# Kernel tuning notes

Measured on AMD Instinct MI355X. Metric: run time of the kernel, lower is better.

## Reference

```python
import jax, jax.numpy as jnp
import numpy as np

TAU = 0.75

def normalize_W(W):
    n = jnp.linalg.norm(W)
    n = jax.nn.relu(n - 1.0) + 1.0
    return W / n

def setup_inputs() -> dict:
    key = jax.random.key(0)
    ks = jax.random.split(key, 14)
    C_in, C_out, K = 64, 128, 3
    B, L = 32, 4096
    nh = 64
    chunk_in_d = C_out * K            # 384
    D = C_in * (K + 2 * (C_out // C_in))  # 448
    r = lambda k, shp, s=1.0: jax.random.normal(k, shp, dtype=jnp.float32) * s
    W = normalize_W(r(ks[4], (D, 32)))
    return {
        "x": r(ks[0], (B, C_in, L)),
        "conv_weight": r(ks[1], (C_out, C_in, K), 0.1),
        "bias_param": r(ks[2], (C_out,), 0.1),
        "grads": r(ks[3], (C_out * C_in * K,), 0.1),
        "W": W,
        "ctrl_w": r(ks[5], (nh, chunk_in_d), 0.05),
        "ctrl_b": r(ks[6], (nh,), 0.05),
        "cw_w": r(ks[7], (K, nh), 0.05),
        "cw_b": r(ks[8], (K,), 0.05),
        "cb_w": r(ks[9], (C_out // C_in, nh), 0.05),
        "cb_b": r(ks[10], (C_out // C_in,), 0.05),
        "cf_w": r(ks[11], (C_out // C_in, nh), 0.05),
        "cf_b": r(ks[12], (C_out // C_in,), 0.05),
        "trigger": 1,
    }

def fw_chunks(grads, W, ctrl_w, ctrl_b, cw_w, cw_b, cb_w, cb_b, cf_w, cf_b, trigger, n_chunks):
    g = grads.reshape(n_chunks, -1)                    # (C_in, C_out*K)
    rep = jax.nn.silu(g @ ctrl_w.T + ctrl_b)           # (C_in, nh)
    w = rep @ cw_w.T + cw_b                            # (C_in, K)
    b = rep @ cb_w.T + cb_b                            # (C_in, C_out/C_in)
    f = rep @ cf_w.T + cf_b                            # (C_in, C_out/C_in)
    q = jnp.concatenate([w.ravel(), b.ravel(), f.ravel()])  # (D,)  first call: no q_ema
    W_upd = W
    if trigger == 1:  # codebook attention / top-k / scatter-EMA path
        dim = w.shape[0]
        att = jax.nn.softmax(q @ W / 0.5)              # (32,)
        v, idx = jax.lax.top_k(att, 2)
        ww = W[:, idx]                                 # (D, 2)
        old_w = ww @ idx.astype(jnp.float32)[:, None]  # (D, 1) -- indices used as weights, as in source
        s_att = jnp.zeros((att.shape[0],), jnp.float32).at[idx].set(v)
        W_contrib = old_w @ s_att[None, :]             # (D, 32)
        mask = jnp.ones(W.shape, jnp.float32).at[:, idx].set(TAU)
        W_upd = normalize_W(mask * W + (1.0 - mask) * W_contrib)
        nw, nb, nf = w.shape[1], b.shape[1], f.shape[1]
        o_w = old_w[: nw * dim]
        o_b = old_w[nw * dim : (nw + nb) * dim]
        o_f = old_w[-nf * dim :]
        w = TAU * w + (1.0 - TAU) * o_w.reshape(w.shape)
        b = TAU * b + (1.0 - TAU) * o_b.reshape(b.shape)
        f = TAU * f + (1.0 - TAU) * o_f.reshape(f.shape)
    f = f.reshape(-1)[None, :, None]                   # (1, C_out, 1)
    return w[None], b.reshape(-1), f, W_upd

def reference(x, conv_weight, bias_param, grads, W, ctrl_w, ctrl_b, cw_w, cw_b, cb_w, cb_b, cf_w, cf_b, trigger):
    n_chunks = conv_weight.shape[1]  # in_channels
    w, b, f, W_upd = fw_chunks(grads, W, ctrl_w, ctrl_b, cw_w, cw_b, cb_w, cb_b, cf_w, cf_b, trigger, n_chunks)
    cw = conv_weight * w                               # (C_out, C_in, K)
    pad = ((conv_weight.shape[2] - 1) * 1 + 1) // 2    # receptive_field // 2
    conv_out = jax.lax.conv_general_dilated(
        x, cw, window_strides=(1,), padding=[(pad, pad)], rhs_dilation=(1,),
        dimension_numbers=("NCH", "OIH", "NCH"))
    conv_out = conv_out + (bias_param * b)[None, :, None]
    out = f * conv_out                                 # (B, C_out, L)
    return out, W_upd
```

## Files before the change

### kernel.cpp

```cpp
#include <hip/hip_runtime.h>
#include <hip/hip_bf16.h>
#include <math.h>

#define TAU 0.75f

typedef _Float16 half8 __attribute__((ext_vector_type(8)));
typedef float    f32x4 __attribute__((ext_vector_type(4)));

#define LDS_BARRIER() do {                                   \
    asm volatile("s_waitcnt lgkmcnt(0)" ::: "memory");       \
    __builtin_amdgcn_s_barrier();                            \
    asm volatile("" ::: "memory");                           \
} while (0)

#define WS_Q     0
#define WS_NORM2 448
#define WS_SCALE 449
#define WS_V01   450
#define WS_I01   452
#define WS_WQ    456
#define WS_FSC   648
#define WS_BADD  776
#define WS_OW    904
#define WS_WF16  1352

__global__ __launch_bounds__(256) void k1_rep_q(
    const float* __restrict__ grads, const float* __restrict__ ctrl_w,
    const float* __restrict__ ctrl_b,
    const float* __restrict__ cw_w, const float* __restrict__ cw_b,
    const float* __restrict__ cb_w, const float* __restrict__ cb_b,
    const float* __restrict__ cf_w, const float* __restrict__ cf_b,
    const float* __restrict__ W, float* __restrict__ ws)
{
    const int t = threadIdx.x;
    if (blockIdx.x == 64) {
        __shared__ float red[256];
        float ss = 0.f;
        for (int e = t; e < 3584; e += 256) {
            const float4 w4 = ((const float4*)W)[e];
            ss += w4.x * w4.x + w4.y * w4.y + w4.z * w4.z + w4.w * w4.w;
        }
        red[t] = ss; __syncthreads();
        for (int s = 128; s > 0; s >>= 1) { if (t < s) red[t] += red[t + s]; __syncthreads(); }
        if (t == 0) ws[WS_NORM2] = red[0];
        return;
    }
    const int c = blockIdx.x;
    __shared__ float gS[384];
    __shared__ float repS[64];
    if (t < 96) ((float4*)gS)[t] = ((const float4*)(grads + c * 384))[t];
    __syncthreads();
    {
        const int h = t >> 2, sub = t & 3;
        const float4* wa = (const float4*)(ctrl_w + h * 384) + sub * 24;
        const float4* ga = (const float4*)gS + sub * 24;
        float dot = 0.f;
        #pragma unroll
        for (int d = 0; d < 24; d++) {
            const float4 a = ga[d], b = wa[d];
            dot += a.x * b.x + a.y * b.y + a.z * b.z + a.w * b.w;
        }
        dot += __shfl_xor(dot, 1);
        dot += __shfl_xor(dot, 2);
        if (sub == 0) {
            const float z = dot + ctrl_b[h];
            repS[h] = z / (1.f + expf(-z));
        }
    }
    __syncthreads();
    if (t < 7) {
        const float* wv; float bias; int e;
        if (t < 3)      { wv = cw_w + t * 64;       bias = cw_b[t];     e = 3 * c + t; }
        else if (t < 5) { const int j = t - 3; wv = cb_w + j * 64; bias = cb_b[j]; e = 192 + 2 * c + j; }
        else            { const int j = t - 5; wv = cf_w + j * 64; bias = cf_b[j]; e = 320 + 2 * c + j; }
        float dot = 0.f;
        #pragma unroll 8
        for (int h = 0; h < 64; h++) dot += repS[h] * wv[h];
        ws[WS_Q + e] = dot + bias;
    }
}

__global__ __launch_bounds__(256) void k2_small(
    const float* __restrict__ W, const float* __restrict__ bias_param,
    const int* __restrict__ trigger, float* __restrict__ ws)
{
    __shared__ float qS[448], owS[448], sS[32], sW[4][32], red[256];
    __shared__ int   idxS[2];
    __shared__ float vS[2];
    const int t = threadIdx.x;
    const int wv = t >> 6, lane = t & 63;
    const int trig = trigger[0];

    for (int e = t; e < 448; e += 256) qS[e] = ws[WS_Q + e];
    __syncthreads();

    {
        const int m = lane & 31, half = lane >> 5;
        float s = 0.f;
        const int base = wv * 112;
        #pragma unroll 4
        for (int it = 0; it < 56; it++) {
            const int d = base + it * 2 + half;
            s += qS[d] * W[d * 32 + m];
        }
        s += __shfl_xor(s, 32);
        if (lane < 32) sW[wv][lane] = s;
    }
    __syncthreads();
    if (t < 32) sS[t] = 2.f * (sW[0][t] + sW[1][t] + sW[2][t] + sW[3][t]);
    __syncthreads();
    if (t == 0) {
        float mx = sS[0];
        for (int m = 1; m < 32; m++) mx = fmaxf(mx, sS[m]);
        float sum = 0.f; float att[32];
        for (int m = 0; m < 32; m++) { att[m] = expf(sS[m] - mx); sum += att[m]; }
        const float inv = 1.f / sum;
        int i0 = 0; float v0 = att[0];
        for (int m = 1; m < 32; m++) if (att[m] > v0) { v0 = att[m]; i0 = m; }
        int i1 = -1; float v1 = -1.f;
        for (int m = 0; m < 32; m++) { if (m == i0) continue; if (att[m] > v1) { v1 = att[m]; i1 = m; } }
        idxS[0] = i0; idxS[1] = i1; vS[0] = v0 * inv; vS[1] = v1 * inv;
    }
    __syncthreads();
    const int i0 = idxS[0], i1 = idxS[1];
    const float v0 = vS[0], v1 = vS[1];

    float corr = 0.f;
    for (int d = t; d < 448; d += 256) {
        const float w0 = W[d * 32 + i0], w1 = W[d * 32 + i1];
        const float ow = (trig == 1) ? (w0 * (float)i0 + w1 * (float)i1) : 0.f;
        owS[d] = ow;
        if (trig == 1) {
            const float n0 = TAU * w0 + 0.25f * ow * v0;
            const float n1 = TAU * w1 + 0.25f * ow * v1;
            corr += n0 * n0 - w0 * w0 + n1 * n1 - w1 * w1;
        }
    }
    red[t] = corr; __syncthreads();
    for (int s = 128; s > 0; s >>= 1) { if (t < s) red[t] += red[t + s]; __syncthreads(); }
    if (t == 0) {
        const float n = sqrtf(fmaxf(ws[WS_NORM2] + red[0], 0.f));
        ws[WS_SCALE] = 1.f / fmaxf(n, 1.f);
        ws[WS_V01] = v0; ws[WS_V01 + 1] = v1;
        ((int*)ws)[WS_I01] = i0; ((int*)ws)[WS_I01 + 1] = i1;
    }

    if (t < 192) ws[WS_WQ + t] = (trig == 1) ? (TAU * qS[t] + 0.25f * owS[t]) : qS[t];
    for (int o = t; o < 128; o += 256) {
        float bb = qS[192 + o], ff = qS[320 + o];
        if (trig == 1) {
            bb = TAU * bb + 0.25f * owS[192 + o];
            ff = TAU * ff + 0.25f * owS[320 + o];
        }
        ws[WS_FSC + o]  = ff;
        ws[WS_BADD + o] = ff * bias_param[o] * bb;
    }
    for (int d = t; d < 448; d += 256) ws[WS_OW + d] = owS[d];
}

__global__ __launch_bounds__(256) void k3_finalize(
    const float* __restrict__ W, const float* __restrict__ conv_weight,
    const int* __restrict__ trigger, const float* __restrict__ ws,
    float* __restrict__ W_out, _Float16* __restrict__ wf_out)
{
    const int g = blockIdx.x * 256 + threadIdx.x;
    const int trig = trigger[0];
    if (g < 14336) {
        const float wv = W[g];
        float wn = wv;
        if (trig == 1) {
            const int d = g >> 5, m = g & 31;
            const int i0 = ((const int*)ws)[WS_I01], i1 = ((const int*)ws)[WS_I01 + 1];
            if (m == i0)      wn = TAU * wv + 0.25f * ws[WS_OW + d] * ws[WS_V01];
            else if (m == i1) wn = TAU * wv + 0.25f * ws[WS_OW + d] * ws[WS_V01 + 1];
            wn *= ws[WS_SCALE];
        }
        W_out[g] = wn;
    } else {
        const int e2 = g - 14336;
        const int o   = e2 / 192;
        const int rem = e2 - o * 192;
        const int i   = rem / 3;
        const int kk  = rem - i * 3;
        wf_out[(kk * 128 + o) * 64 + i] = (_Float16)(conv_weight[e2] * ws[WS_WQ + rem]);
    }
}

__global__ __launch_bounds__(256, 4) void conv_mfma(
    const float* __restrict__ x, const _Float16* __restrict__ wf,
    const float* __restrict__ fsc, const float* __restrict__ badd,
    float* __restrict__ out)
{
    __shared__ __align__(16) _Float16 xs[2][66 * 72];

    const int t    = threadIdx.x;
    const int wv   = t >> 6;
    const int lane = t & 63;
    const int lrow = lane & 15;
    const int lgrp = lane >> 4;
    const int b    = blockIdx.x >> 5;
    const int l0   = (blockIdx.x & 31) * 128;
    const int obase = wv * 32;

    const float* xb = x + (size_t)b * 64 * 4096;
    const int ci = t & 3;
    const int ir = t >> 2;
    const int ei = t & 63;
    const int side = (t >> 6) & 1;

    half8 Wf[2][2][3];
    #pragma unroll
    for (int of = 0; of < 2; of++)
        #pragma unroll
        for (int ch = 0; ch < 2; ch++)
            #pragma unroll
            for (int kk = 0; kk < 3; kk++)
                Wf[of][ch][kk] = *(const half8*)(wf + ((kk * 128 + obase + of * 16 + lrow) * 64 + ch * 32 + lgrp * 8));

    float4 xr0[4]; float xe0 = 0.f;
    float4 xr1[4]; float xe1 = 0.f;

    {
        const int lb = l0;
        #pragma unroll
        for (int j = 0; j < 4; j++)
            xr0[j] = *(const float4*)(xb + (size_t)ir * 4096 + lb + ci * 16 + j * 4);
        if (t < 128) {
            const int l = side ? (lb + 64) : (lb - 1);
            if (l >= 0 && l < 4096) xe0 = xb[(size_t)ei * 4096 + l];
        }
    }
    {
        _Float16* buf = xs[0];
        #pragma unroll
        for (int j = 0; j < 4; j++) {
            _Float16* p = buf + (ci * 16 + j * 4 + 1) * 72 + ir;
            p[0]   = (_Float16)xr0[j].x;
            p[72]  = (_Float16)xr0[j].y;
            p[144] = (_Float16)xr0[j].z;
            p[216] = (_Float16)xr0[j].w;
        }
        if (t < 128) buf[(side ? 65 : 0) * 72 + ei] = (_Float16)xe0;
    }
    {
        const int lb = l0 + 64;
        #pragma unroll
        for (int j = 0; j < 4; j++)
            xr1[j] = *(const float4*)(xb + (size_t)ir * 4096 + lb + ci * 16 + j * 4);
        if (t < 128) {
            const int l = side ? (lb + 64) : (lb - 1);
            if (l >= 0 && l < 4096) xe1 = xb[(size_t)ei * 4096 + l];
        }
    }
    LDS_BARRIER();

    #pragma unroll
    for (int tile = 0; tile < 2; tile++) {
        const _Float16* buf = xs[tile];
        const int lb = l0 + tile * 64;

        f32x4 acc[2][4];
        #pragma unroll
        for (int of = 0; of < 2; of++)
            #pragma unroll
            for (int lf = 0; lf < 4; lf++) acc[of][lf] = (f32x4)0.f;

        #pragma unroll
        for (int ch = 0; ch < 2; ch++) {
            #pragma unroll
            for (int kk = 0; kk < 3; kk++) {
                half8 Xf[4];
                #pragma unroll
                for (int lf = 0; lf < 4; lf++)
                    Xf[lf] = *(const half8*)(buf + (lf * 16 + lrow + kk) * 72 + ch * 32 + lgrp * 8);
                #pragma unroll
                for (int of = 0; of < 2; of++)
                    #pragma unroll
                    for (int lf = 0; lf < 4; lf++)
                        acc[of][lf] = __builtin_amdgcn_mfma_f32_16x16x32_f16(Xf[lf], Wf[of][ch][kk], acc[of][lf], 0, 0, 0);
            }
        }

        #pragma unroll
        for (int of = 0; of < 2; of++) {
            const int o = obase + of * 16 + lrow;
            const float fs = fsc[o], ba = badd[o];
            float* orow = out + ((size_t)(b * 128 + o)) * 4096 + lb + lgrp * 4;
            #pragma unroll
            for (int lf = 0; lf < 4; lf++) {
                float4 r;
                r.x = fs * acc[of][lf][0] + ba;
                r.y = fs * acc[of][lf][1] + ba;
                r.z = fs * acc[of][lf][2] + ba;
                r.w = fs * acc[of][lf][3] + ba;
                *(float4*)(orow + lf * 16) = r;
            }
        }

        if (tile == 0) {
            _Float16* buf1 = xs[1];
            #pragma unroll
            for (int j = 0; j < 4; j++) {
                _Float16* p = buf1 + (ci * 16 + j * 4 + 1) * 72 + ir;
                p[0]   = (_Float16)xr1[j].x;
                p[72]  = (_Float16)xr1[j].y;
                p[144] = (_Float16)xr1[j].z;
                p[216] = (_Float16)xr1[j].w;
            }
            if (t < 128) buf1[(side ? 65 : 0) * 72 + ei] = (_Float16)xe1;
            LDS_BARRIER();
        }
    }
}

extern "C" void kernel_launch(void* const* d_in, const int* in_sizes, int n_in,
                              void* d_out, int out_size, void* d_ws, size_t ws_size,
                              hipStream_t stream) {
    const float* x           = (const float*)d_in[0];
    const float* conv_weight = (const float*)d_in[1];
    const float* bias_param  = (const float*)d_in[2];
    const float* grads       = (const float*)d_in[3];
    const float* W           = (const float*)d_in[4];
    const float* ctrl_w      = (const float*)d_in[5];
    const float* ctrl_b      = (const float*)d_in[6];
    const float* cw_w        = (const float*)d_in[7];
    const float* cw_b        = (const float*)d_in[8];
    const float* cb_w        = (const float*)d_in[9];
    const float* cb_b        = (const float*)d_in[10];
    const float* cf_w        = (const float*)d_in[11];
    const float* cf_b        = (const float*)d_in[12];
    const int*   trigger     = (const int*)d_in[13];

    float* out   = (float*)d_out;
    float* W_out = out + (size_t)32 * 128 * 4096;
    float* ws    = (float*)d_ws;
    _Float16* wfp = (_Float16*)(ws + WS_WF16);
    float* fsc   = ws + WS_FSC;
    float* badd  = ws + WS_BADD;

    k1_rep_q<<<65, 256, 0, stream>>>(grads, ctrl_w, ctrl_b, cw_w, cw_b,
                                     cb_w, cb_b, cf_w, cf_b, W, ws);
    k2_small<<<1, 256, 0, stream>>>(W, bias_param, trigger, ws);
    k3_finalize<<<152, 256, 0, stream>>>(W, conv_weight, trigger, ws, W_out, wfp);
    conv_mfma<<<1024, 256, 0, stream>>>(x, wfp, fsc, badd, out);
}
```

Measured before the change: 46.51 us.

## Process four L-tiles per conv block with a rolling double-buffered LDS pipeline

Each conv block now covers 256 positions (four 64-wide tiles) instead of 128, and the grid is halved to 512 blocks. A ping-pong pipeline loads the next tile's x from global memory into registers while the current tile is computed, then writes it to the other LDS buffer. The fsc/badd loads are hoisted out of the tile loop. The aim is to amortise the per-block weight-fragment loads and prologue, at the cost of fewer blocks (launch bound lowered to 2) and more registers, which may reduce occupancy and latency hiding on a bandwidth-bound kernel.

```diff
diff --git a/kernel.cpp b/kernel.cpp
--- a/kernel.cpp
+++ b/kernel.cpp
@@ -186,20 +186,20 @@
     }
 }
 
-__global__ __launch_bounds__(256, 4) void conv_mfma(
+__global__ __launch_bounds__(256, 2) void conv_mfma(
     const float* __restrict__ x, const _Float16* __restrict__ wf,
     const float* __restrict__ fsc, const float* __restrict__ badd,
     float* __restrict__ out)
 {
     __shared__ __align__(16) _Float16 xs[2][66 * 72];
 
-    const int t    = threadIdx.x;
-    const int wv   = t >> 6;
-    const int lane = t & 63;
-    const int lrow = lane & 15;
-    const int lgrp = lane >> 4;
-    const int b    = blockIdx.x >> 5;
-    const int l0   = (blockIdx.x & 31) * 128;
+    const int t     = threadIdx.x;
+    const int wv    = t >> 6;
+    const int lane  = t & 63;
+    const int lrow  = lane & 15;
+    const int lgrp  = lane >> 4;
+    const int b     = blockIdx.x >> 4;
+    const int lbase = (blockIdx.x & 15) * 256;
     const int obase = wv * 32;
 
     const float* xb = x + (size_t)b * 64 * 4096;
@@ -217,100 +217,100 @@
             for (int kk = 0; kk < 3; kk++)
                 Wf[of][ch][kk] = *(const half8*)(wf + ((kk * 128 + obase + of * 16 + lrow) * 64 + ch * 32 + lgrp * 8));
 
-    float4 xr0[4]; float xe0 = 0.f;
-    float4 xr1[4]; float xe1 = 0.f;
-
-    {
-        const int lb = l0;
-        #pragma unroll
-        for (int j = 0; j < 4; j++)
-            xr0[j] = *(const float4*)(xb + (size_t)ir * 4096 + lb + ci * 16 + j * 4);
-        if (t < 128) {
-            const int l = side ? (lb + 64) : (lb - 1);
-            if (l >= 0 && l < 4096) xe0 = xb[(size_t)ei * 4096 + l];
-        }
-    }
-    {
-        _Float16* buf = xs[0];
-        #pragma unroll
-        for (int j = 0; j < 4; j++) {
-            _Float16* p = buf + (ci * 16 + j * 4 + 1) * 72 + ir;
-            p[0]   = (_Float16)xr0[j].x;
-            p[72]  = (_Float16)xr0[j].y;
-            p[144] = (_Float16)xr0[j].z;
-            p[216] = (_Float16)xr0[j].w;
-        }
-        if (t < 128) buf[(side ? 65 : 0) * 72 + ei] = (_Float16)xe0;
-    }
-    {
-        const int lb = l0 + 64;
-        #pragma unroll
-        for (int j = 0; j < 4; j++)
-            xr1[j] = *(const float4*)(xb + (size_t)ir * 4096 + lb + ci * 16 + j * 4);
-        if (t < 128) {
-            const int l = side ? (lb + 64) : (lb - 1);
-            if (l >= 0 && l < 4096) xe1 = xb[(size_t)ei * 4096 + l];
-        }
-    }
+    float fs_[2], ba_[2];
+    #pragma unroll
+    for (int of = 0; of < 2; of++) {
+        const int o = obase + of * 16 + lrow;
+        fs_[of] = fsc[o]; ba_[of] = badd[o];
+    }
+
+    float4 xrA[4], xrB[4];
+    float  xeA = 0.f, xeB = 0.f;
+
+#define STAGE_LOAD(xr, xe, lb) do {                                          \
+    _Pragma("unroll")                                                        \
+    for (int j = 0; j < 4; j++)                                              \
+        (xr)[j] = *(const float4*)(xb + (size_t)ir * 4096 + (lb) + ci * 16 + j * 4); \
+    (xe) = 0.f;                                                              \
+    if (t < 128) {                                                           \
+        const int l_ = side ? ((lb) + 64) : ((lb) - 1);                      \
+        if (l_ >= 0 && l_ < 4096) (xe) = xb[(size_t)ei * 4096 + l_];         \
+    }                                                                        \
+} while (0)
+
+#define STAGE_WRITE(buf, xr, xe) do {                                        \
+    _Pragma("unroll")                                                        \
+    for (int j = 0; j < 4; j++) {                                            \
+        _Float16* p_ = (buf) + (ci * 16 + j * 4 + 1) * 72 + ir;              \
+        p_[0]   = (_Float16)(xr)[j].x;                                       \
+        p_[72]  = (_Float16)(xr)[j].y;                                       \
+        p_[144] = (_Float16)(xr)[j].z;                                       \
+        p_[216] = (_Float16)(xr)[j].w;                                       \
+    }                                                                        \
+    if (t < 128) (buf)[(side ? 65 : 0) * 72 + ei] = (_Float16)(xe);          \
+} while (0)
+
+#define COMPUTE_STORE(buf, lb) do {                                          \
+    f32x4 acc[2][4];                                                         \
+    _Pragma("unroll")                                                        \
+    for (int of = 0; of < 2; of++)                                           \
+        _Pragma("unroll")                                                    \
+        for (int lf = 0; lf < 4; lf++) acc[of][lf] = (f32x4)0.f;             \
+    _Pragma("unroll")                                                        \
+    for (int ch = 0; ch < 2; ch++) {                                         \
+        _Pragma("unroll")                                                    \
+        for (int kk = 0; kk < 3; kk++) {                                     \
+            half8 Xf[4];                                                     \
+            _Pragma("unroll")                                                \
+            for (int lf = 0; lf < 4; lf++)                                   \
+                Xf[lf] = *(const half8*)((buf) + (lf * 16 + lrow + kk) * 72 + ch * 32 + lgrp * 8); \
+            _Pragma("unroll")                                                \
+            for (int of = 0; of < 2; of++)                                   \
+                _Pragma("unroll")                                            \
+                for (int lf = 0; lf < 4; lf++)                               \
+                    acc[of][lf] = __builtin_amdgcn_mfma_f32_16x16x32_f16(Xf[lf], Wf[of][ch][kk], acc[of][lf], 0, 0, 0); \
+        }                                                                    \
+    }                                                                        \
+    _Pragma("unroll")                                                        \
+    for (int of = 0; of < 2; of++) {                                         \
+        const int o_ = obase + of * 16 + lrow;                               \
+        float* orow_ = out + ((size_t)(b * 128 + o_)) * 4096 + (lb) + lgrp * 4; \
+        _Pragma("unroll")                                                    \
+        for (int lf = 0; lf < 4; lf++) {                                     \
+            float4 r_;                                                       \
+            r_.x = fs_[of] * acc[of][lf][0] + ba_[of];                       \
+            r_.y = fs_[of] * acc[of][lf][1] + ba_[of];                       \
+            r_.z = fs_[of] * acc[of][lf][2] + ba_[of];                       \
+            r_.w = fs_[of] * acc[of][lf][3] + ba_[of];                       \
+            *(float4*)(orow_ + lf * 16) = r_;                                \
+        }                                                                    \
+    }                                                                        \
+} while (0)
+
+    STAGE_LOAD(xrA, xeA, lbase);
+    STAGE_WRITE(xs[0], xrA, xeA);
+    STAGE_LOAD(xrB, xeB, lbase + 64);
     LDS_BARRIER();
 
-    #pragma unroll
-    for (int tile = 0; tile < 2; tile++) {
-        const _Float16* buf = xs[tile];
-        const int lb = l0 + tile * 64;
-
-        f32x4 acc[2][4];
-        #pragma unroll
-        for (int of = 0; of < 2; of++)
-            #pragma unroll
-            for (int lf = 0; lf < 4; lf++) acc[of][lf] = (f32x4)0.f;
-
-        #pragma unroll
-        for (int ch = 0; ch < 2; ch++) {
-            #pragma unroll
-            for (int kk = 0; kk < 3; kk++) {
-                half8 Xf[4];
-                #pragma unroll
-                for (int lf = 0; lf < 4; lf++)
-                    Xf[lf] = *(const half8*)(buf + (lf * 16 + lrow + kk) * 72 + ch * 32 + lgrp * 8);
-                #pragma unroll
-                for (int of = 0; of < 2; of++)
-                    #pragma unroll
-                    for (int lf = 0; lf < 4; lf++)
-                        acc[of][lf] = __builtin_amdgcn_mfma_f32_16x16x32_f16(Xf[lf], Wf[of][ch][kk], acc[of][lf], 0, 0, 0);
-            }
-        }
-
-        #pragma unroll
-        for (int of = 0; of < 2; of++) {
-            const int o = obase + of * 16 + lrow;
-            const float fs = fsc[o], ba = badd[o];
-            float* orow = out + ((size_t)(b * 128 + o)) * 4096 + lb + lgrp * 4;
-            #pragma unroll
-            for (int lf = 0; lf < 4; lf++) {
-                float4 r;
-                r.x = fs * acc[of][lf][0] + ba;
-                r.y = fs * acc[of][lf][1] + ba;
-                r.z = fs * acc[of][lf][2] + ba;
-                r.w = fs * acc[of][lf][3] + ba;
-                *(float4*)(orow + lf * 16) = r;
-            }
-        }
-
-        if (tile == 0) {
-            _Float16* buf1 = xs[1];
-            #pragma unroll
-            for (int j = 0; j < 4; j++) {
-                _Float16* p = buf1 + (ci * 16 + j * 4 + 1) * 72 + ir;
-                p[0]   = (_Float16)xr1[j].x;
-                p[72]  = (_Float16)xr1[j].y;
-                p[144] = (_Float16)xr1[j].z;
-                p[216] = (_Float16)xr1[j].w;
-            }
-            if (t < 128) buf1[(side ? 65 : 0) * 72 + ei] = (_Float16)xe1;
-            LDS_BARRIER();
-        }
-    }
+    STAGE_LOAD(xrA, xeA, lbase + 128);
+    COMPUTE_STORE(xs[0], lbase);
+    STAGE_WRITE(xs[1], xrB, xeB);
+    LDS_BARRIER();
+
+    STAGE_LOAD(xrB, xeB, lbase + 192);
+    COMPUTE_STORE(xs[1], lbase + 64);
+    STAGE_WRITE(xs[0], xrA, xeA);
+    LDS_BARRIER();
+
+    COMPUTE_STORE(xs[0], lbase + 128);
+    STAGE_WRITE(xs[1], xrB, xeB);
+    LDS_BARRIER();
+
+    COMPUTE_STORE(xs[1], lbase + 192);
+
+#undef STAGE_LOAD
+#undef STAGE_WRITE
+#undef COMPUTE_STORE
 }
 
 extern "C" void kernel_launch(void* const* d_in, const int* in_sizes, int n_in,
@@ -342,5 +342,5 @@
                                      cb_w, cb_b, cf_w, cf_b, W, ws);
     k2_small<<<1, 256, 0, stream>>>(W, bias_param, trigger, ws);
     k3_finalize<<<152, 256, 0, stream>>>(W, conv_weight, trigger, ws, W_out, wfp);
-    conv_mfma<<<1024, 256, 0, stream>>>(x, wfp, fsc, badd, out);
-}
+    conv_mfma<<<512, 256, 0, stream>>>(x, wfp, fsc, badd, out);
+}
```

After: 41.85 us, median of 2. 10.0% less time.

## Restructure conv so each wave owns a 64-position tile and all output channels

Applied to the files above, without the earlier changes.

The conv kernel now gives each wave its own 64-position slice of x in a private LDS buffer with an XOR swizzle. Each wave computes all 128 output channels, streaming weight fragments from global/L2 instead of holding them in registers, and the block barriers are removed. The per-channel f scale is folded into the fp16 weights in the finalize kernel, and the grid drops to 512 blocks of 256 positions. The accumulator grows to 128 floats per lane, so occupancy is lower and weight loads are repeated for every MFMA group.

```diff
diff --git a/kernel.cpp b/kernel.cpp
--- a/kernel.cpp
+++ b/kernel.cpp
@@ -7,11 +7,7 @@
 typedef _Float16 half8 __attribute__((ext_vector_type(8)));
 typedef float    f32x4 __attribute__((ext_vector_type(4)));
 
-#define LDS_BARRIER() do {                                   \
-    asm volatile("s_waitcnt lgkmcnt(0)" ::: "memory");       \
-    __builtin_amdgcn_s_barrier();                            \
-    asm volatile("" ::: "memory");                           \
-} while (0)
+#define SWZ(row) ((((row) >> 3) & 7) << 3)
 
 #define WS_Q     0
 #define WS_NORM2 448
@@ -182,133 +178,87 @@
         const int rem = e2 - o * 192;
         const int i   = rem / 3;
         const int kk  = rem - i * 3;
-        wf_out[(kk * 128 + o) * 64 + i] = (_Float16)(conv_weight[e2] * ws[WS_WQ + rem]);
-    }
-}
-
-__global__ __launch_bounds__(256, 4) void conv_mfma(
+        wf_out[(kk * 128 + o) * 64 + i] =
+            (_Float16)(conv_weight[e2] * ws[WS_WQ + rem] * ws[WS_FSC + o]);
+    }
+}
+
+__global__ __launch_bounds__(256, 2) void conv_mfma(
     const float* __restrict__ x, const _Float16* __restrict__ wf,
-    const float* __restrict__ fsc, const float* __restrict__ badd,
-    float* __restrict__ out)
-{
-    __shared__ __align__(16) _Float16 xs[2][66 * 72];
+    const float* __restrict__ badd, float* __restrict__ out)
+{
+    __shared__ __align__(16) _Float16 xs[4][66 * 72];
 
     const int t    = threadIdx.x;
     const int wv   = t >> 6;
     const int lane = t & 63;
     const int lrow = lane & 15;
     const int lgrp = lane >> 4;
-    const int b    = blockIdx.x >> 5;
-    const int l0   = (blockIdx.x & 31) * 128;
-    const int obase = wv * 32;
+    const int b    = blockIdx.x >> 4;
+    const int lb   = (blockIdx.x & 15) * 256 + wv * 64;
 
     const float* xb = x + (size_t)b * 64 * 4096;
-    const int ci = t & 3;
-    const int ir = t >> 2;
-    const int ei = t & 63;
-    const int side = (t >> 6) & 1;
-
-    half8 Wf[2][2][3];
+    _Float16* buf = xs[wv];
+
+    {
+        const int i = lane;
+        const float* xr = xb + (size_t)i * 4096 + lb;
+        #pragma unroll
+        for (int j = 0; j < 16; j++) {
+            const float4 v = *(const float4*)(xr + j * 4);
+            const int c0 = j * 4 + 1;
+            buf[(c0 + 0) * 72 + (i ^ SWZ(c0 + 0))] = (_Float16)v.x;
+            buf[(c0 + 1) * 72 + (i ^ SWZ(c0 + 1))] = (_Float16)v.y;
+            buf[(c0 + 2) * 72 + (i ^ SWZ(c0 + 2))] = (_Float16)v.z;
+            buf[(c0 + 3) * 72 + (i ^ SWZ(c0 + 3))] = (_Float16)v.w;
+        }
+        float xl = 0.f, xh = 0.f;
+        if (lb > 0)        xl = xr[-1];
+        if (lb + 64 < 4096) xh = xr[64];
+        buf[0 * 72 + (i ^ SWZ(0))]   = (_Float16)xl;
+        buf[65 * 72 + (i ^ SWZ(65))] = (_Float16)xh;
+    }
+
+    f32x4 acc[8][4];
     #pragma unroll
-    for (int of = 0; of < 2; of++)
-        #pragma unroll
-        for (int ch = 0; ch < 2; ch++)
+    for (int of = 0; of < 8; of++)
+        #pragma unroll
+        for (int lf = 0; lf < 4; lf++) acc[of][lf] = (f32x4)0.f;
+
+    #pragma unroll
+    for (int ch = 0; ch < 2; ch++) {
+        #pragma unroll
+        for (int kk = 0; kk < 3; kk++) {
+            half8 Xf[4];
             #pragma unroll
-            for (int kk = 0; kk < 3; kk++)
-                Wf[of][ch][kk] = *(const half8*)(wf + ((kk * 128 + obase + of * 16 + lrow) * 64 + ch * 32 + lgrp * 8));
-
-    float4 xr0[4]; float xe0 = 0.f;
-    float4 xr1[4]; float xe1 = 0.f;
-
-    {
-        const int lb = l0;
-        #pragma unroll
-        for (int j = 0; j < 4; j++)
-            xr0[j] = *(const float4*)(xb + (size_t)ir * 4096 + lb + ci * 16 + j * 4);
-        if (t < 128) {
-            const int l = side ? (lb + 64) : (lb - 1);
-            if (l >= 0 && l < 4096) xe0 = xb[(size_t)ei * 4096 + l];
-        }
-    }
-    {
-        _Float16* buf = xs[0];
-        #pragma unroll
-        for (int j = 0; j < 4; j++) {
-            _Float16* p = buf + (ci * 16 + j * 4 + 1) * 72 + ir;
-            p[0]   = (_Float16)xr0[j].x;
-            p[72]  = (_Float16)xr0[j].y;
-            p[144] = (_Float16)xr0[j].z;
-            p[216] = (_Float16)xr0[j].w;
-        }
-        if (t < 128) buf[(side ? 65 : 0) * 72 + ei] = (_Float16)xe0;
-    }
-    {
-        const int lb = l0 + 64;
-        #pragma unroll
-        for (int j = 0; j < 4; j++)
-            xr1[j] = *(const float4*)(xb + (size_t)ir * 4096 + lb + ci * 16 + j * 4);
-        if (t < 128) {
-            const int l = side ? (lb + 64) : (lb - 1);
-            if (l >= 0 && l < 4096) xe1 = xb[(size_t)ei * 4096 + l];
-        }
-    }
-    LDS_BARRIER();
-
-    #pragma unroll
-    for (int tile = 0; tile < 2; tile++) {
-        const _Float16* buf = xs[tile];
-        const int lb = l0 + tile * 64;
-
-        f32x4 acc[2][4];
-        #pragma unroll
-        for (int of = 0; of < 2; of++)
+            for (int lf = 0; lf < 4; lf++) {
+                const int rr = lf * 16 + lrow + kk;
+                Xf[lf] = *(const half8*)(buf + rr * 72 + ((ch * 32 + lgrp * 8) ^ SWZ(rr)));
+            }
             #pragma unroll
-            for (int lf = 0; lf < 4; lf++) acc[of][lf] = (f32x4)0.f;
-
-        #pragma unroll
-        for (int ch = 0; ch < 2; ch++) {
-            #pragma unroll
-            for (int kk = 0; kk < 3; kk++) {
-                half8 Xf[4];
+            for (int of = 0; of < 8; of++) {
+                const half8 Wfv = *(const half8*)(wf +
+                    ((kk * 128 + of * 16 + lrow) * 64 + ch * 32 + lgrp * 8));
                 #pragma unroll
                 for (int lf = 0; lf < 4; lf++)
-                    Xf[lf] = *(const half8*)(buf + (lf * 16 + lrow + kk) * 72 + ch * 32 + lgrp * 8);
-                #pragma unroll
-                for (int of = 0; of < 2; of++)
-                    #pragma unroll
-                    for (int lf = 0; lf < 4; lf++)
-                        acc[of][lf] = __builtin_amdgcn_mfma_f32_16x16x32_f16(Xf[lf], Wf[of][ch][kk], acc[of][lf], 0, 0, 0);
+                    acc[of][lf] = __builtin_amdgcn_mfma_f32_16x16x32_f16(Xf[lf], Wfv, acc[of][lf], 0, 0, 0);
             }
         }
-
-        #pragma unroll
-        for (int of = 0; of < 2; of++) {
-            const int o = obase + of * 16 + lrow;
-            const float fs = fsc[o], ba = badd[o];
-            float* orow = out + ((size_t)(b * 128 + o)) * 4096 + lb + lgrp * 4;
-            #pragma unroll
-            for (int lf = 0; lf < 4; lf++) {
-                float4 r;
-                r.x = fs * acc[of][lf][0] + ba;
-                r.y = fs * acc[of][lf][1] + ba;
-                r.z = fs * acc[of][lf][2] + ba;
-                r.w = fs * acc[of][lf][3] + ba;
-                *(float4*)(orow + lf * 16) = r;
-            }
-        }
-
-        if (tile == 0) {
-            _Float16* buf1 = xs[1];
-            #pragma unroll
-            for (int j = 0; j < 4; j++) {
-                _Float16* p = buf1 + (ci * 16 + j * 4 + 1) * 72 + ir;
-                p[0]   = (_Float16)xr1[j].x;
-                p[72]  = (_Float16)xr1[j].y;
-                p[144] = (_Float16)xr1[j].z;
-                p[216] = (_Float16)xr1[j].w;
-            }
-            if (t < 128) buf1[(side ? 65 : 0) * 72 + ei] = (_Float16)xe1;
-            LDS_BARRIER();
+    }
+
+    #pragma unroll
+    for (int of = 0; of < 8; of++) {
+        const int o = of * 16 + lrow;
+        const float ba = badd[o];
+        float* orow = out + ((size_t)(b * 128 + o)) * 4096 + lb + lgrp * 4;
+        #pragma unroll
+        for (int lf = 0; lf < 4; lf++) {
+            float4 r;
+            r.x = acc[of][lf][0] + ba;
+            r.y = acc[of][lf][1] + ba;
+            r.z = acc[of][lf][2] + ba;
+            r.w = acc[of][lf][3] + ba;
+            *(float4*)(orow + lf * 16) = r;
         }
     }
 }
@@ -335,12 +285,11 @@
     float* W_out = out + (size_t)32 * 128 * 4096;
     float* ws    = (float*)d_ws;
     _Float16* wfp = (_Float16*)(ws + WS_WF16);
-    float* fsc   = ws + WS_FSC;
     float* badd  = ws + WS_BADD;
 
     k1_rep_q<<<65, 256, 0, stream>>>(grads, ctrl_w, ctrl_b, cw_w, cw_b,
                                      cb_w, cb_b, cf_w, cf_b, W, ws);
     k2_small<<<1, 256, 0, stream>>>(W, bias_param, trigger, ws);
     k3_finalize<<<152, 256, 0, stream>>>(W, conv_weight, trigger, ws, W_out, wfp);
-    conv_mfma<<<1024, 256, 0, stream>>>(x, wfp, fsc, badd, out);
-}
+    conv_mfma<<<512, 256, 0, stream>>>(x, wfp, badd, out);
+}
```

New measurement: 50.18 us. 7.9% more time.
